# Kernel optimization log

Measured on AMD Instinct MI355X. Metric: run time of the kernel, lower is better.

The kernel has to match this reference:

```python
import jax, jax.numpy as jnp
import numpy as np

B, L, G, H = 16384, 4096, 30000, 256
LN_EPS = 1e-5


def setup_inputs() -> dict:
    key = jax.random.key(0)
    k0, k1, k2, k3 = jax.random.split(key, 4)
    x = jax.random.uniform(k0, (B, L), dtype=jnp.float32)          # cell x gene expression
    gene_idx = jax.random.randint(k1, (L,), 0, G)                   # irregular gene indices
    emb = jax.random.normal(k2, (G, H), dtype=jnp.float32) * 0.005  # gene embedding table
    W1 = jax.random.normal(k3, (H, H), dtype=jnp.float32) * (1.0 / np.sqrt(H))
    b1 = jnp.zeros((H,), dtype=jnp.float32)
    gamma = jnp.ones((H,), dtype=jnp.float32)
    beta = jnp.zeros((H,), dtype=jnp.float32)
    return {"x": x, "emb": emb, "W1": W1, "b1": b1, "gamma": gamma,
            "beta": beta, "gene_idx": gene_idx}


def reference(x, emb, W1, b1, gamma, beta, gene_idx):
    # OmicsEmbedder: gather gene embeddings, then weighted aggregation per cell
    feat = emb[gene_idx]                     # [L, H]  F.embedding gather
    h = x @ feat                             # [B, H]  torch.sparse.mm(x, feat)
    # extra_linear: Linear -> ReLU -> Dropout(eval: identity) -> LayerNorm
    h = jax.nn.relu(h @ W1 + b1)             # [B, H]
    mu = jnp.mean(h, axis=-1, keepdims=True)
    var = jnp.mean(jnp.square(h - mu), axis=-1, keepdims=True)
    return gamma * (h - mu) * jax.lax.rsqrt(var + LN_EPS) + beta
```

## Files before the change

### kernel.cpp

```cpp
#include <hip/hip_runtime.h>
#include <stdint.h>

#define B_DIM 16384
#define L_DIM 4096
#define H_DIM 256
#define LN_EPS 1e-5f

typedef unsigned short u16;
typedef __attribute__((ext_vector_type(4))) float f32x4;
typedef __attribute__((ext_vector_type(8))) short short8;

__device__ __forceinline__ u16 f2bf(float f) {
  union { float f; uint32_t u; } v; v.f = f;
  uint32_t u = v.u;
  u += 0x7FFFu + ((u >> 16) & 1u);
  return (u16)(u >> 16);
}

__device__ __forceinline__ void gload_lds16(const void* g, void* l) {
  __builtin_amdgcn_global_load_lds((const __attribute__((address_space(1))) void*)g,
                                   (__attribute__((address_space(3))) void*)l, 16, 0, 0);
}

__global__ __launch_bounds__(256) void prep_frag(const float* __restrict__ emb,
                                                 const int* __restrict__ gidx,
                                                 u16* __restrict__ fragB) {
  const int t = threadIdx.x;
  const int l = t & 63;
  const int w = t >> 6;
  const int frag = blockIdx.x * 4 + w;
  const int kstep = frag >> 4;
  const int nt = frag & 15;
  const int n = nt * 16 + (l & 15);
  const int kbase = kstep * 32 + (l >> 4) * 8;
  short8 v;
#pragma unroll
  for (int j = 0; j < 8; ++j) {
    const int g = gidx[kbase + j];
    v[j] = (short)f2bf(emb[(size_t)g * H_DIM + n]);
  }
  *reinterpret_cast<short8*>(fragB + ((size_t)frag * 64 + l) * 8) = v;
}

__global__ __launch_bounds__(256) void prep_tr(const float* __restrict__ src,
                                               const int* __restrict__ idx,
                                               u16* __restrict__ dst,
                                               int Ktot, int srcW) {
  __shared__ u16 tile[64][66];
  const int t = threadIdx.x;
  const int k0 = blockIdx.x * 64;
  const int n0 = blockIdx.y * 64;
  for (int r0 = 0; r0 < 64; r0 += 4) {
    const int kk = k0 + r0 + (t >> 6);
    const int nn = n0 + (t & 63);
    const int srow = idx ? idx[kk] : kk;
    tile[r0 + (t >> 6)][t & 63] = f2bf(src[(size_t)srow * srcW + nn]);
  }
  __syncthreads();
  for (int c = t; c < 512; c += 256) {
    const int n = c >> 3;
    const int inner = c & 7;
    const int nG = n0 + n;
    short8 v;
#pragma unroll
    for (int j = 0; j < 8; ++j) v[j] = (short)tile[inner * 8 + j][n];
    const size_t didx = (size_t)nG * Ktot + (size_t)k0 +
                        (size_t)((inner * 8) ^ ((nG & 7) << 3));
    *reinterpret_cast<short8*>(dst + didx) = v;
  }
}

__global__ __launch_bounds__(256, 2) void gemm1(const float* __restrict__ x,
                                                const u16* __restrict__ fragB,
                                                u16* __restrict__ h_s) {
  __shared__ __align__(16) char pool[81920];
  const int t = threadIdx.x;
  const int l = t & 63;
  const int w = t >> 6;
  const int wm = w >> 1;
  const int wk = w & 1;
  const int m0 = blockIdx.x * 32;
  const float* xbase = x + (size_t)m0 * L_DIM;

  f32x4 acc[16] = {};

#pragma unroll
  for (int i = 0; i < 2; ++i) {
    const int R = (w * 2 + i) * 4 + (l >> 4);
    const int c16 = (l & 15) ^ ((R & 7) << 1);
    gload_lds16(xbase + (size_t)R * L_DIM + c16 * 4,
                pool + 65536 + (w * 2 + i) * 1024);
  }
#pragma unroll
  for (int i = 0; i < 8; ++i) {
    const int j = w * 8 + i;
    gload_lds16(fragB + ((size_t)((j >> 4) * 16 + (j & 15)) * 64 + l) * 8,
                pool + j * 1024);
  }

  for (int s = 0; s < 64; ++s) {
    asm volatile("s_waitcnt vmcnt(0)" ::: "memory");
    __builtin_amdgcn_s_barrier();
    __builtin_amdgcn_sched_barrier(0);
    if (s < 63) {
      const int nx = s + 1, nb = nx & 1;
#pragma unroll
      for (int i = 0; i < 2; ++i) {
        const int R = (w * 2 + i) * 4 + (l >> 4);
        const int c16 = (l & 15) ^ ((R & 7) << 1);
        gload_lds16(xbase + (size_t)R * L_DIM + nx * 64 + c16 * 4,
                    pool + 65536 + nb * 8192 + (w * 2 + i) * 1024);
      }
      const u16* srcB = fragB + (size_t)(nx * 2) * 16 * 512;
#pragma unroll
      for (int i = 0; i < 8; ++i) {
        const int j = w * 8 + i;
        gload_lds16(srcB + ((size_t)((j >> 4) * 16 + (j & 15)) * 64 + l) * 8,
                    pool + nb * 32768 + j * 1024);
      }
    }
    const int cb = s & 1;
    const int row = wm * 16 + (l & 15);
    const int abyte = (wk * 128 + (l >> 4) * 32) ^ ((row & 7) << 5);
    const float* ap = (const float*)(pool + 65536 + cb * 8192 + row * 256 + abyte);
    const float4 a0 = *(const float4*)ap;
    const float4 a1 = *(const float4*)(ap + 4);
    short8 af;
    af[0] = (short)f2bf(a0.x); af[1] = (short)f2bf(a0.y);
    af[2] = (short)f2bf(a0.z); af[3] = (short)f2bf(a0.w);
    af[4] = (short)f2bf(a1.x); af[5] = (short)f2bf(a1.y);
    af[6] = (short)f2bf(a1.z); af[7] = (short)f2bf(a1.w);
    const u16* bb = (const u16*)(pool + cb * 32768) + (wk * 16) * 512 + l * 8;
#pragma unroll
    for (int nt = 0; nt < 16; ++nt) {
      const short8 bf = *reinterpret_cast<const short8*>(bb + nt * 512);
      acc[nt] = __builtin_amdgcn_mfma_f32_16x16x32_bf16(af, bf, acc[nt], 0, 0, 0);
    }
    asm volatile("s_waitcnt lgkmcnt(0)" ::: "memory");
    __builtin_amdgcn_s_barrier();
  }

  float* red = (float*)pool;
  __syncthreads();
  if (wk == 1) {
#pragma unroll
    for (int nt = 0; nt < 16; ++nt)
#pragma unroll
      for (int r = 0; r < 4; ++r)
        red[(wm * 16 + (l >> 4) * 4 + r) * 260 + nt * 16 + (l & 15)] = acc[nt][r];
  }
  __syncthreads();
  if (wk == 0) {
#pragma unroll
    for (int r = 0; r < 4; ++r) {
      const int row_l = wm * 16 + (l >> 4) * 4 + r;
      const int row_g = m0 + row_l;
      const int swz = (row_g & 7) << 3;
      u16* hp = h_s + (size_t)row_g * H_DIM;
#pragma unroll
      for (int nt = 0; nt < 16; ++nt) {
        const int col = nt * 16 + (l & 15);
        hp[col ^ swz] = f2bf(acc[nt][r] + red[row_l * 260 + col]);
      }
    }
  }
}

__global__ __launch_bounds__(256, 1) void gemm2_ln(const u16* __restrict__ h_s,
                                                   const u16* __restrict__ w1T,
                                                   const float* __restrict__ b1,
                                                   const float* __restrict__ gmm,
                                                   const float* __restrict__ bta,
                                                   float* __restrict__ out) {
  __shared__ __align__(16) u16 As[64 * 64];
  __shared__ __align__(16) u16 Bs[256 * 64];
  __shared__ float red_s[4][64];
  __shared__ float red_q[4][64];
  __shared__ float mean_s[64];
  __shared__ float rstd_s[64];
  const int t = threadIdx.x;
  const int lane = t & 63;
  const int w = t >> 6;
  const int m0 = blockIdx.x * 64;
  const int bn = t >> 3;
  const int binner = (t & 7) * 8;

  f32x4 acc[4][4] = {};
  for (int kt = 0; kt < 4; ++kt) {
    __syncthreads();
#pragma unroll
    for (int r = 0; r < 2; ++r) {
      const u16* gp = h_s + (size_t)(m0 + r * 32 + bn) * H_DIM + kt * 64 + binner;
      gload_lds16(gp, &As[(r * 256 + w * 64) * 8]);
    }
#pragma unroll
    for (int r = 0; r < 8; ++r) {
      const u16* gp = w1T + (size_t)(r * 32 + bn) * H_DIM + kt * 64 + binner;
      gload_lds16(gp, &Bs[(r * 256 + w * 64) * 8]);
    }
    __syncthreads();
#pragma unroll
    for (int ks = 0; ks < 2; ++ks) {
      const int kb = ks * 64 + ((lane >> 4) * 16);
      short8 af[4], bf[4];
#pragma unroll
      for (int mi = 0; mi < 4; ++mi) {
        const int row = mi * 16 + (lane & 15);
        af[mi] = *reinterpret_cast<const short8*>(
            reinterpret_cast<const char*>(As) + row * 128 + (kb ^ ((row & 7) << 4)));
      }
#pragma unroll
      for (int ni = 0; ni < 4; ++ni) {
        const int n = w * 64 + ni * 16 + (lane & 15);
        bf[ni] = *reinterpret_cast<const short8*>(
            reinterpret_cast<const char*>(Bs) + n * 128 + (kb ^ ((n & 7) << 4)));
      }
#pragma unroll
      for (int mi = 0; mi < 4; ++mi)
#pragma unroll
        for (int ni = 0; ni < 4; ++ni)
          acc[mi][ni] = __builtin_amdgcn_mfma_f32_16x16x32_bf16(af[mi], bf[ni], acc[mi][ni], 0, 0, 0);
    }
  }
  const int cbase = w * 64 + (lane & 15);
  float cb[4];
#pragma unroll
  for (int ni = 0; ni < 4; ++ni) cb[ni] = b1[cbase + ni * 16];
#pragma unroll
  for (int mi = 0; mi < 4; ++mi)
#pragma unroll
    for (int ni = 0; ni < 4; ++ni)
#pragma unroll
      for (int r = 0; r < 4; ++r)
        acc[mi][ni][r] = fmaxf(acc[mi][ni][r] + cb[ni], 0.0f);
#pragma unroll
  for (int mi = 0; mi < 4; ++mi) {
#pragma unroll
    for (int r = 0; r < 4; ++r) {
      float s = 0.f, q = 0.f;
#pragma unroll
      for (int ni = 0; ni < 4; ++ni) { const float v = acc[mi][ni][r]; s += v; q += v * v; }
#pragma unroll
      for (int msk = 1; msk < 16; msk <<= 1) { s += __shfl_xor(s, msk); q += __shfl_xor(q, msk); }
      if ((lane & 15) == 0) {
        const int row = mi * 16 + (lane >> 4) * 4 + r;
        red_s[w][row] = s;
        red_q[w][row] = q;
      }
    }
  }
  __syncthreads();
  if (t < 64) {
    const float s = red_s[0][t] + red_s[1][t] + red_s[2][t] + red_s[3][t];
    const float q = red_q[0][t] + red_q[1][t] + red_q[2][t] + red_q[3][t];
    const float mu = s * (1.0f / 256.0f);
    const float var = q * (1.0f / 256.0f) - mu * mu;
    mean_s[t] = mu;
    rstd_s[t] = rsqrtf(var + LN_EPS);
  }
  __syncthreads();
  float cg[4], cbt[4];
#pragma unroll
  for (int ni = 0; ni < 4; ++ni) { cg[ni] = gmm[cbase + ni * 16]; cbt[ni] = bta[cbase + ni * 16]; }
#pragma unroll
  for (int mi = 0; mi < 4; ++mi) {
#pragma unroll
    for (int r = 0; r < 4; ++r) {
      const int row = mi * 16 + (lane >> 4) * 4 + r;
      const float mu = mean_s[row];
      const float rs = rstd_s[row];
      float* op = out + (size_t)(m0 + row) * H_DIM;
#pragma unroll
      for (int ni = 0; ni < 4; ++ni)
        op[cbase + ni * 16] = cg[ni] * (acc[mi][ni][r] - mu) * rs + cbt[ni];
    }
  }
}

extern "C" void kernel_launch(void* const* d_in, const int* in_sizes, int n_in,
                              void* d_out, int out_size, void* d_ws, size_t ws_size,
                              hipStream_t stream) {
  const float* x    = (const float*)d_in[0];
  const float* emb  = (const float*)d_in[1];
  const float* W1   = (const float*)d_in[2];
  const float* b1   = (const float*)d_in[3];
  const float* gmm  = (const float*)d_in[4];
  const float* bta  = (const float*)d_in[5];
  const int*   gidx = (const int*)d_in[6];
  float* out = (float*)d_out;

  char* ws = (char*)d_ws;
  u16* fragB = (u16*)ws;
  u16* w1T   = (u16*)(ws + (size_t)H_DIM * L_DIM * 2);
  u16* h_s   = (u16*)(ws + (size_t)H_DIM * L_DIM * 2
                          + (size_t)H_DIM * H_DIM * 2);

  prep_frag<<<512, 256, 0, stream>>>(emb, gidx, fragB);
  prep_tr<<<dim3(H_DIM / 64, H_DIM / 64), 256, 0, stream>>>(W1, nullptr, w1T, H_DIM, H_DIM);
  gemm1<<<dim3(B_DIM / 32), 256, 0, stream>>>(x, fragB, h_s);
  gemm2_ln<<<dim3(B_DIM / 64), 256, 0, stream>>>(h_s, w1T, b1, gmm, bta, out);
}
```

Measured before the change: 123.3 us.

## Fuse both GEMMs and LayerNorm into one kernel with triple-buffered x pipeline

```diff
diff --git a/kernel.cpp b/kernel.cpp
--- a/kernel.cpp
+++ b/kernel.cpp
@@ -5,6 +5,7 @@
 #define L_DIM 4096
 #define H_DIM 256
 #define LN_EPS 1e-5f
+#define PERM4(r) ((((r) & 7) << 1) | (((r) >> 3) & 1))
 
 typedef unsigned short u16;
 typedef __attribute__((ext_vector_type(4))) float f32x4;
@@ -22,9 +23,9 @@
                                    (__attribute__((address_space(3))) void*)l, 16, 0, 0);
 }
 
-__global__ __launch_bounds__(256) void prep_frag(const float* __restrict__ emb,
-                                                 const int* __restrict__ gidx,
-                                                 u16* __restrict__ fragB) {
+__global__ __launch_bounds__(256) void prep_frag(const float* __restrict__ src,
+                                                 const int* __restrict__ idx,
+                                                 u16* __restrict__ dst) {
   const int t = threadIdx.x;
   const int l = t & 63;
   const int w = t >> 6;
@@ -36,243 +37,198 @@
   short8 v;
 #pragma unroll
   for (int j = 0; j < 8; ++j) {
-    const int g = gidx[kbase + j];
-    v[j] = (short)f2bf(emb[(size_t)g * H_DIM + n]);
-  }
-  *reinterpret_cast<short8*>(fragB + ((size_t)frag * 64 + l) * 8) = v;
-}
-
-__global__ __launch_bounds__(256) void prep_tr(const float* __restrict__ src,
-                                               const int* __restrict__ idx,
-                                               u16* __restrict__ dst,
-                                               int Ktot, int srcW) {
-  __shared__ u16 tile[64][66];
-  const int t = threadIdx.x;
-  const int k0 = blockIdx.x * 64;
-  const int n0 = blockIdx.y * 64;
-  for (int r0 = 0; r0 < 64; r0 += 4) {
-    const int kk = k0 + r0 + (t >> 6);
-    const int nn = n0 + (t & 63);
-    const int srow = idx ? idx[kk] : kk;
-    tile[r0 + (t >> 6)][t & 63] = f2bf(src[(size_t)srow * srcW + nn]);
-  }
-  __syncthreads();
-  for (int c = t; c < 512; c += 256) {
-    const int n = c >> 3;
-    const int inner = c & 7;
-    const int nG = n0 + n;
-    short8 v;
-#pragma unroll
-    for (int j = 0; j < 8; ++j) v[j] = (short)tile[inner * 8 + j][n];
-    const size_t didx = (size_t)nG * Ktot + (size_t)k0 +
-                        (size_t)((inner * 8) ^ ((nG & 7) << 3));
-    *reinterpret_cast<short8*>(dst + didx) = v;
-  }
-}
-
-__global__ __launch_bounds__(256, 2) void gemm1(const float* __restrict__ x,
+    const int k = kbase + j;
+    const int g = idx ? idx[k] : k;
+    v[j] = (short)f2bf(src[(size_t)g * H_DIM + n]);
+  }
+  *reinterpret_cast<short8*>(dst + ((size_t)frag * 64 + l) * 8) = v;
+}
+
+__global__ __launch_bounds__(512, 2) void fused(const float* __restrict__ x,
                                                 const u16* __restrict__ fragB,
-                                                u16* __restrict__ h_s) {
-  __shared__ __align__(16) char pool[81920];
+                                                const u16* __restrict__ fragW,
+                                                const float* __restrict__ b1,
+                                                const float* __restrict__ gmm,
+                                                const float* __restrict__ bta,
+                                                float* __restrict__ out) {
+  __shared__ __align__(16) char pool[114688];
   const int t = threadIdx.x;
   const int l = t & 63;
   const int w = t >> 6;
   const int wm = w >> 1;
-  const int wk = w & 1;
-  const int m0 = blockIdx.x * 32;
+  const int wn = w & 1;
+  const int m0 = blockIdx.x * 64;
   const float* xbase = x + (size_t)m0 * L_DIM;
-
-  f32x4 acc[16] = {};
+  char* const bufA = pool + 65536;
 
 #pragma unroll
   for (int i = 0; i < 2; ++i) {
     const int R = (w * 2 + i) * 4 + (l >> 4);
-    const int c16 = (l & 15) ^ ((R & 7) << 1);
-    gload_lds16(xbase + (size_t)R * L_DIM + c16 * 4,
-                pool + 65536 + (w * 2 + i) * 1024);
-  }
-#pragma unroll
-  for (int i = 0; i < 8; ++i) {
-    const int j = w * 8 + i;
-    gload_lds16(fragB + ((size_t)((j >> 4) * 16 + (j & 15)) * 64 + l) * 8,
-                pool + j * 1024);
-  }
+    const int c16 = (l & 15) ^ PERM4(R);
+    gload_lds16(xbase + (size_t)R * L_DIM + c16 * 4, bufA + (w * 2 + i) * 1024);
+  }
+  __builtin_amdgcn_sched_barrier(0);
+#pragma unroll
+  for (int i = 0; i < 4; ++i) {
+    const int j = w * 4 + i;
+    gload_lds16(fragB + (size_t)j * 512 + l * 8, pool + j * 1024);
+  }
+  __builtin_amdgcn_sched_barrier(0);
+#pragma unroll
+  for (int i = 0; i < 2; ++i) {
+    const int R = (w * 2 + i) * 4 + (l >> 4);
+    const int c16 = (l & 15) ^ PERM4(R);
+    gload_lds16(xbase + (size_t)R * L_DIM + 64 + c16 * 4,
+                bufA + 16384 + (w * 2 + i) * 1024);
+  }
+  __builtin_amdgcn_sched_barrier(0);
+
+  f32x4 acc[8] = {};
+  const int arow = wm * 16 + (l & 15);
+  const int p4 = PERM4(arow);
 
   for (int s = 0; s < 64; ++s) {
-    asm volatile("s_waitcnt vmcnt(0)" ::: "memory");
+    if (s == 63) asm volatile("s_waitcnt vmcnt(0)" ::: "memory");
+    else         asm volatile("s_waitcnt vmcnt(2)" ::: "memory");
     __builtin_amdgcn_s_barrier();
     __builtin_amdgcn_sched_barrier(0);
     if (s < 63) {
-      const int nx = s + 1, nb = nx & 1;
+      const u16* srcB = fragB + (size_t)(s + 1) * 32 * 512;
+#pragma unroll
+      for (int i = 0; i < 4; ++i) {
+        const int j = w * 4 + i;
+        gload_lds16(srcB + (size_t)j * 512 + l * 8,
+                    pool + ((s + 1) & 1) * 32768 + j * 1024);
+      }
+    }
+    __builtin_amdgcn_sched_barrier(0);
+    if (s < 62) {
+      const int nx = s + 2;
 #pragma unroll
       for (int i = 0; i < 2; ++i) {
         const int R = (w * 2 + i) * 4 + (l >> 4);
-        const int c16 = (l & 15) ^ ((R & 7) << 1);
+        const int c16 = (l & 15) ^ PERM4(R);
         gload_lds16(xbase + (size_t)R * L_DIM + nx * 64 + c16 * 4,
-                    pool + 65536 + nb * 8192 + (w * 2 + i) * 1024);
-      }
-      const u16* srcB = fragB + (size_t)(nx * 2) * 16 * 512;
-#pragma unroll
-      for (int i = 0; i < 8; ++i) {
-        const int j = w * 8 + i;
-        gload_lds16(srcB + ((size_t)((j >> 4) * 16 + (j & 15)) * 64 + l) * 8,
-                    pool + nb * 32768 + j * 1024);
-      }
-    }
-    const int cb = s & 1;
-    const int row = wm * 16 + (l & 15);
-    const int abyte = (wk * 128 + (l >> 4) * 32) ^ ((row & 7) << 5);
-    const float* ap = (const float*)(pool + 65536 + cb * 8192 + row * 256 + abyte);
-    const float4 a0 = *(const float4*)ap;
-    const float4 a1 = *(const float4*)(ap + 4);
-    short8 af;
-    af[0] = (short)f2bf(a0.x); af[1] = (short)f2bf(a0.y);
-    af[2] = (short)f2bf(a0.z); af[3] = (short)f2bf(a0.w);
-    af[4] = (short)f2bf(a1.x); af[5] = (short)f2bf(a1.y);
-    af[6] = (short)f2bf(a1.z); af[7] = (short)f2bf(a1.w);
-    const u16* bb = (const u16*)(pool + cb * 32768) + (wk * 16) * 512 + l * 8;
-#pragma unroll
-    for (int nt = 0; nt < 16; ++nt) {
-      const short8 bf = *reinterpret_cast<const short8*>(bb + nt * 512);
-      acc[nt] = __builtin_amdgcn_mfma_f32_16x16x32_bf16(af, bf, acc[nt], 0, 0, 0);
+                    bufA + (nx % 3) * 16384 + (w * 2 + i) * 1024);
+      }
+    }
+    __builtin_amdgcn_sched_barrier(0);
+    const char* bA = bufA + (s % 3) * 16384;
+    const char* bB = pool + (s & 1) * 32768;
+#pragma unroll
+    for (int ks = 0; ks < 2; ++ks) {
+      const int gs = ks * 8 + (l >> 4) * 2;
+      const float4 a0 = *(const float4*)(bA + arow * 256 + ((gs ^ p4) * 16));
+      const float4 a1 = *(const float4*)(bA + arow * 256 + (((gs + 1) ^ p4) * 16));
+      short8 af;
+      af[0] = (short)f2bf(a0.x); af[1] = (short)f2bf(a0.y);
+      af[2] = (short)f2bf(a0.z); af[3] = (short)f2bf(a0.w);
+      af[4] = (short)f2bf(a1.x); af[5] = (short)f2bf(a1.y);
+      af[6] = (short)f2bf(a1.z); af[7] = (short)f2bf(a1.w);
+#pragma unroll
+      for (int nt = 0; nt < 8; ++nt) {
+        const short8 bf = *(const short8*)(bB + (ks * 16 + wn * 8 + nt) * 1024 + l * 16);
+        acc[nt] = __builtin_amdgcn_mfma_f32_16x16x32_bf16(af, bf, acc[nt], 0, 0, 0);
+      }
     }
     asm volatile("s_waitcnt lgkmcnt(0)" ::: "memory");
     __builtin_amdgcn_s_barrier();
   }
 
-  float* red = (float*)pool;
+#pragma unroll
+  for (int i = 0; i < 4; ++i) {
+    const int j = w * 4 + i;
+    gload_lds16(fragW + (size_t)j * 512 + l * 8, pool + j * 1024);
+  }
+  const int hrow_base = wm * 16 + ((l >> 4) << 2);
+#pragma unroll
+  for (int rr = 0; rr < 4; ++rr) {
+    const int row = hrow_base + rr;
+#pragma unroll
+    for (int nt = 0; nt < 8; ++nt) {
+      const int col = wn * 128 + nt * 16 + (l & 15);
+      const int ls = (col >> 3) ^ (row & 15);
+      *(u16*)(bufA + row * 512 + ls * 16 + (col & 7) * 2) = f2bf(acc[nt][rr]);
+    }
+  }
+  asm volatile("s_waitcnt lgkmcnt(0)" ::: "memory");
+  __builtin_amdgcn_s_barrier();
+
+  f32x4 acc2[8] = {};
+  for (int kt = 0; kt < 4; ++kt) {
+    asm volatile("s_waitcnt vmcnt(0)" ::: "memory");
+    __builtin_amdgcn_s_barrier();
+    __builtin_amdgcn_sched_barrier(0);
+    if (kt < 3) {
+      const u16* srcW = fragW + (size_t)(kt + 1) * 32 * 512;
+#pragma unroll
+      for (int i = 0; i < 4; ++i) {
+        const int j = w * 4 + i;
+        gload_lds16(srcW + (size_t)j * 512 + l * 8,
+                    pool + ((kt + 1) & 1) * 32768 + j * 1024);
+      }
+    }
+    __builtin_amdgcn_sched_barrier(0);
+    const char* bW = pool + (kt & 1) * 32768;
+#pragma unroll
+    for (int ksi = 0; ksi < 2; ++ksi) {
+      const int ks = kt * 2 + ksi;
+      const short8 af = *(const short8*)(
+          bufA + arow * 512 + (((ks * 4 + (l >> 4)) ^ (arow & 15)) * 16));
+#pragma unroll
+      for (int nt = 0; nt < 8; ++nt) {
+        const short8 bf = *(const short8*)(bW + (ksi * 16 + wn * 8 + nt) * 1024 + l * 16);
+        acc2[nt] = __builtin_amdgcn_mfma_f32_16x16x32_bf16(af, bf, acc2[nt], 0, 0, 0);
+      }
+    }
+    asm volatile("s_waitcnt lgkmcnt(0)" ::: "memory");
+    __builtin_amdgcn_s_barrier();
+  }
+
+  float bv[8];
+#pragma unroll
+  for (int nt = 0; nt < 8; ++nt) bv[nt] = b1[wn * 128 + nt * 16 + (l & 15)];
+  float s4[4], q4[4];
+#pragma unroll
+  for (int rr = 0; rr < 4; ++rr) {
+    float s = 0.f, q = 0.f;
+#pragma unroll
+    for (int nt = 0; nt < 8; ++nt) {
+      const float v = fmaxf(acc2[nt][rr] + bv[nt], 0.f);
+      acc2[nt][rr] = v; s += v; q += v * v;
+    }
+#pragma unroll
+    for (int m = 1; m < 16; m <<= 1) { s += __shfl_xor(s, m); q += __shfl_xor(q, m); }
+    s4[rr] = s; q4[rr] = q;
+  }
+  float* lnred = (float*)pool;
+  if ((l & 15) == 0) {
+#pragma unroll
+    for (int rr = 0; rr < 4; ++rr) {
+      const int row = hrow_base + rr;
+      lnred[(wn * 64 + row) * 2 + 0] = s4[rr];
+      lnred[(wn * 64 + row) * 2 + 1] = q4[rr];
+    }
+  }
   __syncthreads();
-  if (wk == 1) {
-#pragma unroll
-    for (int nt = 0; nt < 16; ++nt)
-#pragma unroll
-      for (int r = 0; r < 4; ++r)
-        red[(wm * 16 + (l >> 4) * 4 + r) * 260 + nt * 16 + (l & 15)] = acc[nt][r];
-  }
-  __syncthreads();
-  if (wk == 0) {
-#pragma unroll
-    for (int r = 0; r < 4; ++r) {
-      const int row_l = wm * 16 + (l >> 4) * 4 + r;
-      const int row_g = m0 + row_l;
-      const int swz = (row_g & 7) << 3;
-      u16* hp = h_s + (size_t)row_g * H_DIM;
-#pragma unroll
-      for (int nt = 0; nt < 16; ++nt) {
-        const int col = nt * 16 + (l & 15);
-        hp[col ^ swz] = f2bf(acc[nt][r] + red[row_l * 260 + col]);
-      }
-    }
-  }
-}
-
-__global__ __launch_bounds__(256, 1) void gemm2_ln(const u16* __restrict__ h_s,
-                                                   const u16* __restrict__ w1T,
-                                                   const float* __restrict__ b1,
-                                                   const float* __restrict__ gmm,
-                                                   const float* __restrict__ bta,
-                                                   float* __restrict__ out) {
-  __shared__ __align__(16) u16 As[64 * 64];
-  __shared__ __align__(16) u16 Bs[256 * 64];
-  __shared__ float red_s[4][64];
-  __shared__ float red_q[4][64];
-  __shared__ float mean_s[64];
-  __shared__ float rstd_s[64];
-  const int t = threadIdx.x;
-  const int lane = t & 63;
-  const int w = t >> 6;
-  const int m0 = blockIdx.x * 64;
-  const int bn = t >> 3;
-  const int binner = (t & 7) * 8;
-
-  f32x4 acc[4][4] = {};
-  for (int kt = 0; kt < 4; ++kt) {
-    __syncthreads();
-#pragma unroll
-    for (int r = 0; r < 2; ++r) {
-      const u16* gp = h_s + (size_t)(m0 + r * 32 + bn) * H_DIM + kt * 64 + binner;
-      gload_lds16(gp, &As[(r * 256 + w * 64) * 8]);
-    }
-#pragma unroll
-    for (int r = 0; r < 8; ++r) {
-      const u16* gp = w1T + (size_t)(r * 32 + bn) * H_DIM + kt * 64 + binner;
-      gload_lds16(gp, &Bs[(r * 256 + w * 64) * 8]);
-    }
-    __syncthreads();
-#pragma unroll
-    for (int ks = 0; ks < 2; ++ks) {
-      const int kb = ks * 64 + ((lane >> 4) * 16);
-      short8 af[4], bf[4];
-#pragma unroll
-      for (int mi = 0; mi < 4; ++mi) {
-        const int row = mi * 16 + (lane & 15);
-        af[mi] = *reinterpret_cast<const short8*>(
-            reinterpret_cast<const char*>(As) + row * 128 + (kb ^ ((row & 7) << 4)));
-      }
-#pragma unroll
-      for (int ni = 0; ni < 4; ++ni) {
-        const int n = w * 64 + ni * 16 + (lane & 15);
-        bf[ni] = *reinterpret_cast<const short8*>(
-            reinterpret_cast<const char*>(Bs) + n * 128 + (kb ^ ((n & 7) << 4)));
-      }
-#pragma unroll
-      for (int mi = 0; mi < 4; ++mi)
-#pragma unroll
-        for (int ni = 0; ni < 4; ++ni)
-          acc[mi][ni] = __builtin_amdgcn_mfma_f32_16x16x32_bf16(af[mi], bf[ni], acc[mi][ni], 0, 0, 0);
-    }
-  }
-  const int cbase = w * 64 + (lane & 15);
-  float cb[4];
-#pragma unroll
-  for (int ni = 0; ni < 4; ++ni) cb[ni] = b1[cbase + ni * 16];
-#pragma unroll
-  for (int mi = 0; mi < 4; ++mi)
-#pragma unroll
-    for (int ni = 0; ni < 4; ++ni)
-#pragma unroll
-      for (int r = 0; r < 4; ++r)
-        acc[mi][ni][r] = fmaxf(acc[mi][ni][r] + cb[ni], 0.0f);
-#pragma unroll
-  for (int mi = 0; mi < 4; ++mi) {
-#pragma unroll
-    for (int r = 0; r < 4; ++r) {
-      float s = 0.f, q = 0.f;
-#pragma unroll
-      for (int ni = 0; ni < 4; ++ni) { const float v = acc[mi][ni][r]; s += v; q += v * v; }
-#pragma unroll
-      for (int msk = 1; msk < 16; msk <<= 1) { s += __shfl_xor(s, msk); q += __shfl_xor(q, msk); }
-      if ((lane & 15) == 0) {
-        const int row = mi * 16 + (lane >> 4) * 4 + r;
-        red_s[w][row] = s;
-        red_q[w][row] = q;
-      }
-    }
-  }
-  __syncthreads();
-  if (t < 64) {
-    const float s = red_s[0][t] + red_s[1][t] + red_s[2][t] + red_s[3][t];
-    const float q = red_q[0][t] + red_q[1][t] + red_q[2][t] + red_q[3][t];
-    const float mu = s * (1.0f / 256.0f);
-    const float var = q * (1.0f / 256.0f) - mu * mu;
-    mean_s[t] = mu;
-    rstd_s[t] = rsqrtf(var + LN_EPS);
-  }
-  __syncthreads();
-  float cg[4], cbt[4];
-#pragma unroll
-  for (int ni = 0; ni < 4; ++ni) { cg[ni] = gmm[cbase + ni * 16]; cbt[ni] = bta[cbase + ni * 16]; }
-#pragma unroll
-  for (int mi = 0; mi < 4; ++mi) {
-#pragma unroll
-    for (int r = 0; r < 4; ++r) {
-      const int row = mi * 16 + (lane >> 4) * 4 + r;
-      const float mu = mean_s[row];
-      const float rs = rstd_s[row];
-      float* op = out + (size_t)(m0 + row) * H_DIM;
-#pragma unroll
-      for (int ni = 0; ni < 4; ++ni)
-        op[cbase + ni * 16] = cg[ni] * (acc[mi][ni][r] - mu) * rs + cbt[ni];
+  float gg[8], bb[8];
+#pragma unroll
+  for (int nt = 0; nt < 8; ++nt) {
+    const int col = wn * 128 + nt * 16 + (l & 15);
+    gg[nt] = gmm[col]; bb[nt] = bta[col];
+  }
+#pragma unroll
+  for (int rr = 0; rr < 4; ++rr) {
+    const int row = hrow_base + rr;
+    const float S = lnred[row * 2 + 0] + lnred[(64 + row) * 2 + 0];
+    const float Q = lnred[row * 2 + 1] + lnred[(64 + row) * 2 + 1];
+    const float mu = S * (1.0f / 256.0f);
+    const float rstd = rsqrtf(Q * (1.0f / 256.0f) - mu * mu + LN_EPS);
+    float* op = out + (size_t)(m0 + row) * H_DIM;
+#pragma unroll
+    for (int nt = 0; nt < 8; ++nt) {
+      const int col = wn * 128 + nt * 16 + (l & 15);
+      op[col] = gg[nt] * (acc2[nt][rr] - mu) * rstd + bb[nt];
     }
   }
 }
@@ -291,12 +247,9 @@
 
   char* ws = (char*)d_ws;
   u16* fragB = (u16*)ws;
-  u16* w1T   = (u16*)(ws + (size_t)H_DIM * L_DIM * 2);
-  u16* h_s   = (u16*)(ws + (size_t)H_DIM * L_DIM * 2
-                          + (size_t)H_DIM * H_DIM * 2);
+  u16* fragW = (u16*)(ws + (size_t)H_DIM * L_DIM * 2);
 
   prep_frag<<<512, 256, 0, stream>>>(emb, gidx, fragB);
-  prep_tr<<<dim3(H_DIM / 64, H_DIM / 64), 256, 0, stream>>>(W1, nullptr, w1T, H_DIM, H_DIM);
-  gemm1<<<dim3(B_DIM / 32), 256, 0, stream>>>(x, fragB, h_s);
-  gemm2_ln<<<dim3(B_DIM / 64), 256, 0, stream>>>(h_s, w1T, b1, gmm, bta, out);
-}
+  prep_frag<<<32, 256, 0, stream>>>(W1, nullptr, fragW);
+  fused<<<256, 512, 0, stream>>>(x, fragB, fragW, b1, gmm, bta, out);
+}
```

Result: faster. 112.7 us (-8.6%).
